# Kernel tuning notes

Measured on AMD Instinct MI355X. Metric: run time of the kernel, lower is better.

## Reference

```python
import jax, jax.numpy as jnp
import numpy as np

B = 16384      # batch
E = 128        # embed_dim
H = 256        # hidden_dim
OUT = 2        # output_dim
S = 32         # seq_length (decoder steps)
CAR = 8        # car_num


def setup_inputs() -> dict:
    key = jax.random.key(0)
    ks = jax.random.split(key, 17)
    def rn(k, shape, s=0.05):
        return jax.random.normal(k, shape, dtype=jnp.float32) * s
    return {
        "x": rn(ks[0], (B, 6 + CAR * 6), 1.0),
        "emb_mt_W": rn(ks[1], (E, 6)), "emb_mt_b": rn(ks[2], (E,)),
        "emb_v_W": rn(ks[3], (E, 6)), "emb_v_b": rn(ks[4], (E,)),
        "enc_Wih": rn(ks[5], (3 * H, E)), "enc_Whh": rn(ks[6], (3 * H, H)),
        "enc_bih": rn(ks[7], (3 * H,)), "enc_bhh": rn(ks[8], (3 * H,)),
        "dec_Wih": rn(ks[9], (3 * H, H)), "dec_Whh": rn(ks[10], (3 * H, H)),
        "dec_bih": rn(ks[11], (3 * H,)), "dec_bhh": rn(ks[12], (3 * H,)),
        "fc1_W": rn(ks[13], (H, H)), "fc1_b": rn(ks[14], (H,)),
        "fc2_W": rn(ks[15], (OUT, H)), "fc2_b": rn(ks[16], (OUT,)),
    }


def gru_cell(x, h, Wih, Whh, bih, bhh):
    # PyTorch GRU cell: r,z,n gate order
    gi = x @ Wih.T + bih          # [B, 3H]
    gh = h @ Whh.T + bhh          # [B, 3H]
    ir, iz, inn = jnp.split(gi, 3, axis=-1)
    hr, hz, hn = jnp.split(gh, 3, axis=-1)
    r = jax.nn.sigmoid(ir + hr)
    z = jax.nn.sigmoid(iz + hz)
    n = jnp.tanh(inn + r * hn)
    return (1.0 - z) * n + z * h


def reference(x, emb_mt_W, emb_mt_b, emb_v_W, emb_v_b,
              enc_Wih, enc_Whh, enc_bih, enc_bhh,
              dec_Wih, dec_Whh, dec_bih, dec_bhh,
              fc1_W, fc1_b, fc2_W, fc2_b):
    main_target = x[:, :6]                                  # [B,6]
    vehicles = x[:, 6:6 + CAR * 6].reshape(-1, CAR, 6)      # [B,CAR,6]
    # NOTE: original applies a random permutation over the CAR axis
    # (torch.randperm); we use the identity permutation for determinism,
    # the per-element math is identical.
    mt_emb = main_target @ emb_mt_W.T + emb_mt_b            # [B,E]
    v_emb = vehicles @ emb_v_W.T + emb_v_b                  # [B,CAR,E]
    seq = jnp.tanh(jnp.concatenate([v_emb, mt_emb[:, None, :]], axis=1))  # [B,CAR+1,E]

    h0 = jnp.zeros((x.shape[0], H), dtype=x.dtype)
    def enc_step(h, xt):
        return gru_cell(xt, h, enc_Wih, enc_Whh, enc_bih, enc_bhh), None
    h_enc, _ = jax.lax.scan(enc_step, h0, jnp.swapaxes(seq, 0, 1))  # [B,H]

    # decoder_input = encoder_output[:, -1] == final hidden (1-layer GRU)
    def dec_step(carry, _):
        dec_in, h = carry
        h = gru_cell(dec_in, h, dec_Wih, dec_Whh, dec_bih, dec_bhh)
        y = jnp.tanh(jax.nn.relu(h @ fc1_W.T + fc1_b) @ fc2_W.T + fc2_b)  # [B,OUT]
        return (h, h), y
    _, ys = jax.lax.scan(dec_step, (h_enc, h_enc), None, length=S)  # [S,B,OUT]
    return jnp.swapaxes(ys, 0, 1)  # [B,S,OUT]
```

## Files before the change

kernel.cpp:

```cpp
#include <hip/hip_runtime.h>
#include <math.h>
#include <stdint.h>

typedef _Float16 f16;
typedef _Float16 f16x8 __attribute__((ext_vector_type(8)));
typedef float    f32x16 __attribute__((ext_vector_type(16)));

#define NBLK 256
#define NTHR 512
#define MROW 64

#define FC1_F 512
#define FC2_F 640
#define ENC_F 656
#define TOT_F 1232
#define TOT_E (TOT_F*512)

#define MFMA32(a,b,c) __builtin_amdgcn_mfma_f32_32x32x16_f16((a),(b),(c),0,0,0)
#define VMW4()  asm volatile("s_waitcnt vmcnt(4)" ::: "memory")
#define LGKM0() asm volatile("s_waitcnt lgkmcnt(0)" ::: "memory")
#define BARR()  do { __builtin_amdgcn_s_barrier(); asm volatile("" ::: "memory"); } while(0)

__device__ __forceinline__ void gld16(const f16* g, f16* lds){
  __builtin_amdgcn_global_load_lds(
      (const __attribute__((address_space(1))) void*)(uintptr_t)(const void*)g,
      (__attribute__((address_space(3))) void*)(uint32_t)(uintptr_t)(void*)lds,
      16, 0, 0);
}

__device__ __forceinline__ float sigm(float v){
  return __fdividef(1.0f, 1.0f + __expf(-v));
}
__device__ __forceinline__ float tanh_f(float v){
  float t = fminf(v, 8.0f);
  float e = __expf(2.0f * t);
  return 1.0f - 2.0f * __fdividef(1.0f, e + 1.0f);
}
__device__ __forceinline__ int eX(int row, int k){ return row*128 + (k ^ ((row & 7) << 3)); }

__global__ void prep_pack(const float* __restrict__ eWih, const float* __restrict__ eWhh,
                          const float* __restrict__ dWih, const float* __restrict__ dWhh,
                          const float* __restrict__ f1W,  const float* __restrict__ f2W,
                          f16* __restrict__ ws16)
{
  int idx = blockIdx.x * 256 + threadIdx.x;
  if (idx >= TOT_E) return;
  int frag = idx >> 9;
  int lo   = idx & 511;
  int l    = lo >> 3;
  int jj   = lo & 7;
  int c32  = l & 31;
  int half = l >> 5;
  int kin  = half*8 + jj;
  float v = 0.0f;
  if (frag < FC1_F){
    int ct = frag >> 6, st = (frag >> 4) & 3, ks = frag & 15;
    int col = ct*32 + c32, k = ks*16 + kin;
    if      (st == 0) v = dWih[col*256 + k]        + dWhh[col*256 + k];
    else if (st == 1) v = dWih[(256+col)*256 + k]  + dWhh[(256+col)*256 + k];
    else if (st == 2) v = dWih[(512+col)*256 + k];
    else              v = dWhh[(512+col)*256 + k];
  } else if (frag < FC2_F){
    int f = frag - FC1_F, ct = f >> 4, ks = f & 15;
    int col = ct*32 + c32, k = ks*16 + kin;
    v = f1W[col*256 + k];
  } else if (frag < ENC_F){
    int ks = frag - FC2_F, k = ks*16 + kin;
    v = (c32 < 2) ? f2W[c32*256 + k] : 0.0f;
  } else {
    int f = frag - ENC_F, ct = f / 72, r = f % 72;
    int col = ct*32 + c32;
    if (r < 24){ int st = r >> 3, ks = r & 7;  v = eWih[(st*256 + col)*128 + ks*16 + kin]; }
    else { r -= 24; int st = r >> 4, ks = r & 15; v = eWhh[(st*256 + col)*256 + ks*16 + kin]; }
  }
  ws16[idx] = (f16)v;
}

__global__ __launch_bounds__(NTHR, 1)
void fused_net(const float* __restrict__ x,
               const float* __restrict__ emW, const float* __restrict__ emb_,
               const float* __restrict__ evW, const float* __restrict__ evb,
               const float* __restrict__ ebih, const float* __restrict__ ebhh,
               const float* __restrict__ dbih, const float* __restrict__ dbhh,
               const float* __restrict__ f1b, const float* __restrict__ f2b,
               const f16* __restrict__ ws16, float* __restrict__ out)
{
  __shared__ __align__(16) f16 H0[16384];
  __shared__ __align__(16) f16 H1[16384];
  __shared__ __align__(16) f16 stg[32768];
  __shared__ __align__(16) f16 xbuf[8192];

  const int tid  = threadIdx.x;
  const int r0   = blockIdx.x * MROW;
  const int l    = tid & 63;
  const int wu   = __builtin_amdgcn_readfirstlane(tid >> 6);
  const int c32  = l & 31;
  const int half = l >> 5;

  f16* hp = H0;
  f16* hq = H1;

  const int abase = c32*256 + ((half*8) ^ ((l & 7) << 3));
  const int xabase= c32*128 + ((half*8) ^ ((l & 7) << 3));
  const int colm  = wu*32 + c32;

  f16* slot0 = stg + wu*4096;

  const f16* wdecL = ws16 + (size_t)(wu*64)*512          + (size_t)l*8;
  const f16* wfc1L = ws16 + (size_t)(FC1_F + wu*16)*512  + (size_t)l*8;
  const f16* wfc2L = ws16 + (size_t)FC2_F*512            + (size_t)l*8;
  const f16* wencL = ws16 + (size_t)(ENC_F + wu*72)*512  + (size_t)l*8;

  auto enc_issue = [&](int n, int q){
    f16* d = slot0 + q*1024;
    const f16 *g0, *g1;
    if (n < 8)      {                g0 = wencL + (size_t)(     n)*512;  g1 = wencL + (size_t)( 8 + n)*512; }
    else if (n < 24){ int k = n-8;   g0 = wencL + (size_t)(24 + k)*512;  g1 = wencL + (size_t)(40 + k)*512; }
    else if (n < 28){ int j = 2*(n-24); g0 = wencL + (size_t)(16+j)*512; g1 = wencL + (size_t)(17+j)*512; }
    else            { int k = 2*(n-28); g0 = wencL + (size_t)(56+k)*512; g1 = wencL + (size_t)(57+k)*512; }
    gld16(g0, d); gld16(g1, d + 512);
  };
  auto dec_issue = [&](int n, int q){
    f16* d = slot0 + q*1024;
    const f16 *g0, *g1;
    if (n < 16)      {               g0 = wdecL + (size_t)(     n)*512;  g1 = wdecL + (size_t)(16 + n)*512; }
    else if (n < 32) { int k = n-16; g0 = wdecL + (size_t)(32 + k)*512;  g1 = wdecL + (size_t)(48 + k)*512; }
    else             { int f2 = 2*(n-32); g0 = wfc1L + (size_t)f2*512;   g1 = wfc1L + (size_t)(f2+1)*512; }
    gld16(g0, d); gld16(g1, d + 512);
  };

  enc_issue(0, 0); enc_issue(1, 1); enc_issue(2, 2);

  for (int i = tid; i < 16384; i += NTHR) H0[i] = (f16)0.0f;

  {
    const float ebr = ebih[colm]       + ebhh[colm];
    const float ebz = ebih[256 + colm] + ebhh[256 + colm];
    const float ebn = ebih[512 + colm];
    const float ebh = ebhh[512 + colm];

    #pragma unroll 1
    for (int t = 0; t < 9; ++t){
      {
        int e  = tid & 127;
        int rq = tid >> 7;
        const float* Wp = (t < 8) ? (evW + e*6) : (emW + e*6);
        float bb = (t < 8) ? evb[e] : emb_[e];
        float w0 = Wp[0], w1 = Wp[1], w2 = Wp[2], w3 = Wp[3], w4 = Wp[4], w5 = Wp[5];
        int xo = (t < 8) ? (6 + t*6) : 0;
        #pragma unroll 1
        for (int rr = 0; rr < 16; ++rr){
          int row = rq*16 + rr;
          const float* xs = x + (size_t)(r0 + row)*54 + xo;
          float a = bb + xs[0]*w0 + xs[1]*w1 + xs[2]*w2 + xs[3]*w3 + xs[4]*w4 + xs[5]*w5;
          xbuf[eX(row, e)] = (f16)tanh_f(a);
        }
      }
      LGKM0(); BARR();

      f32x16 rvv[2], zvv[2];
      {
        f32x16 aR[2], aZ[2];
        aR[0]=0.f; aR[1]=0.f; aZ[0]=0.f; aZ[1]=0.f;
        #pragma unroll 1
        for (int u = 0; u < 24; ++u){
          VMW4();
          int nn = u + 3;
          if (nn < 36) enc_issue(nn, nn & 3);
          else if (t < 8) enc_issue(nn - 36, nn & 3);
          else dec_issue(nn - 36, nn & 3);
          const f16* sp = slot0 + (u & 3)*1024;
          f16x8 b0 = *(const f16x8*)(sp + l*8);
          f16x8 b1 = *(const f16x8*)(sp + 512 + l*8);
          if (u < 8){
            int ao = xabase ^ (u << 4);
            f16x8 a0 = *(const f16x8*)(xbuf + ao);
            f16x8 a1 = *(const f16x8*)(xbuf + ao + 4096);
            aR[0]=MFMA32(a0,b0,aR[0]); aR[1]=MFMA32(a1,b0,aR[1]);
            aZ[0]=MFMA32(a0,b1,aZ[0]); aZ[1]=MFMA32(a1,b1,aZ[1]);
          } else {
            int ao = abase ^ ((u - 8) << 4);
            f16x8 a0 = *(const f16x8*)(hp + ao);
            f16x8 a1 = *(const f16x8*)(hp + ao + 8192);
            aR[0]=MFMA32(a0,b0,aR[0]); aR[1]=MFMA32(a1,b0,aR[1]);
            aZ[0]=MFMA32(a0,b1,aZ[0]); aZ[1]=MFMA32(a1,b1,aZ[1]);
          }
        }
        #pragma unroll
        for (int rt = 0; rt < 2; ++rt)
          #pragma unroll
          for (int rg = 0; rg < 16; ++rg){
            rvv[rt][rg] = sigm(aR[rt][rg] + ebr);
            zvv[rt][rg] = sigm(aZ[rt][rg] + ebz);
          }
      }
      {
        f32x16 aN[2], aH[2];
        aN[0]=0.f; aN[1]=0.f; aH[0]=0.f; aH[1]=0.f;
        #pragma unroll 1
        for (int m = 0; m < 12; ++m){
          int u = 24 + m;
          VMW4();
          int nn = u + 3;
          if (nn < 36) enc_issue(nn, nn & 3);
          else if (t < 8) enc_issue(nn - 36, nn & 3);
          else dec_issue(nn - 36, nn & 3);
          const f16* sp = slot0 + (u & 3)*1024;
          f16x8 b0 = *(const f16x8*)(sp + l*8);
          f16x8 b1 = *(const f16x8*)(sp + 512 + l*8);
          if (m < 4){
            int j = 2*m;
            int ao0 = xabase ^ (j << 4), ao1 = xabase ^ ((j+1) << 4);
            f16x8 a0 = *(const f16x8*)(xbuf + ao0);
            f16x8 a1 = *(const f16x8*)(xbuf + ao0 + 4096);
            aN[0]=MFMA32(a0,b0,aN[0]); aN[1]=MFMA32(a1,b0,aN[1]);
            f16x8 a2 = *(const f16x8*)(xbuf + ao1);
            f16x8 a3 = *(const f16x8*)(xbuf + ao1 + 4096);
            aN[0]=MFMA32(a2,b1,aN[0]); aN[1]=MFMA32(a3,b1,aN[1]);
          } else {
            int k = 2*(m-4);
            int ao0 = abase ^ (k << 4), ao1 = abase ^ ((k+1) << 4);
            f16x8 a0 = *(const f16x8*)(hp + ao0);
            f16x8 a1 = *(const f16x8*)(hp + ao0 + 8192);
            aH[0]=MFMA32(a0,b0,aH[0]); aH[1]=MFMA32(a1,b0,aH[1]);
            f16x8 a2 = *(const f16x8*)(hp + ao1);
            f16x8 a3 = *(const f16x8*)(hp + ao1 + 8192);
            aH[0]=MFMA32(a2,b1,aH[0]); aH[1]=MFMA32(a3,b1,aH[1]);
          }
        }
        #pragma unroll
        for (int rt = 0; rt < 2; ++rt){
          #pragma unroll
          for (int rg = 0; rg < 16; ++rg){
            int rr  = (rg & 3) + 8*(rg >> 2) + 4*half;
            int row = rt*32 + rr;
            int el  = row*256 + (colm ^ ((rr & 7) << 3));
            float nv = tanh_f(aN[rt][rg] + ebn + rvv[rt][rg]*(aH[rt][rg] + ebh));
            float ho = (float)hp[el];
            hq[el] = (f16)(nv + zvv[rt][rg]*(ho - nv));
          }
        }
      }
      LGKM0(); BARR();
      { f16* tmp = hp; hp = hq; hq = tmp; }
    }
  }

  const float dbr = dbih[colm]       + dbhh[colm];
  const float dbz = dbih[256 + colm] + dbhh[256 + colm];
  const float dbn = dbih[512 + colm];
  const float dbh = dbhh[512 + colm];
  const float f1bb = f1b[colm];
  const float f2bb = (c32 < 2) ? f2b[c32] : 0.0f;

  #pragma unroll 1
  for (int s = 0; s < 32; ++s){
    f32x16 rvv[2], zvv[2];
    {
      f32x16 aR[2], aZ[2];
      aR[0]=0.f; aR[1]=0.f; aZ[0]=0.f; aZ[1]=0.f;
      #pragma unroll 1
      for (int u = 0; u < 16; ++u){
        VMW4();
        int nn = u + 3;
        dec_issue(nn, nn & 3);
        const f16* sp = slot0 + (u & 3)*1024;
        f16x8 b0 = *(const f16x8*)(sp + l*8);
        f16x8 b1 = *(const f16x8*)(sp + 512 + l*8);
        int ao = abase ^ (u << 4);
        f16x8 a0 = *(const f16x8*)(hp + ao);
        f16x8 a1 = *(const f16x8*)(hp + ao + 8192);
        aR[0]=MFMA32(a0,b0,aR[0]); aR[1]=MFMA32(a1,b0,aR[1]);
        aZ[0]=MFMA32(a0,b1,aZ[0]); aZ[1]=MFMA32(a1,b1,aZ[1]);
      }
      #pragma unroll
      for (int rt = 0; rt < 2; ++rt)
        #pragma unroll
        for (int rg = 0; rg < 16; ++rg){
          rvv[rt][rg] = sigm(aR[rt][rg] + dbr);
          zvv[rt][rg] = sigm(aZ[rt][rg] + dbz);
        }
    }
    {
      f32x16 aN[2], aH[2];
      aN[0]=0.f; aN[1]=0.f; aH[0]=0.f; aH[1]=0.f;
      #pragma unroll 1
      for (int u = 16; u < 32; ++u){
        VMW4();
        int nn = u + 3;
        dec_issue(nn, nn & 3);
        const f16* sp = slot0 + (u & 3)*1024;
        f16x8 b0 = *(const f16x8*)(sp + l*8);
        f16x8 b1 = *(const f16x8*)(sp + 512 + l*8);
        int k = u - 16;
        int ao = abase ^ (k << 4);
        f16x8 a0 = *(const f16x8*)(hp + ao);
        f16x8 a1 = *(const f16x8*)(hp + ao + 8192);
        aN[0]=MFMA32(a0,b0,aN[0]); aN[1]=MFMA32(a1,b0,aN[1]);
        aH[0]=MFMA32(a0,b1,aH[0]); aH[1]=MFMA32(a1,b1,aH[1]);
      }
      #pragma unroll
      for (int rt = 0; rt < 2; ++rt){
        #pragma unroll
        for (int rg = 0; rg < 16; ++rg){
          int rr  = (rg & 3) + 8*(rg >> 2) + 4*half;
          int row = rt*32 + rr;
          int el  = row*256 + (colm ^ ((rr & 7) << 3));
          float nv = tanh_f(aN[rt][rg] + dbn + rvv[rt][rg]*(aH[rt][rg] + dbh));
          float ho = (float)hp[el];
          hq[el] = (f16)(nv + zvv[rt][rg]*(ho - nv));
        }
      }
    }
    LGKM0(); BARR();

    {
      f32x16 aF[2];
      aF[0]=0.f; aF[1]=0.f;
      #pragma unroll 1
      for (int f = 0; f < 8; ++f){
        VMW4();
        int nn = 35 + f;
        if (nn < 40) dec_issue(nn, nn & 3);
        else         dec_issue(nn - 40, nn & 3);
        const f16* sp = slot0 + (f & 3)*1024;
        f16x8 b0 = *(const f16x8*)(sp + l*8);
        f16x8 b1 = *(const f16x8*)(sp + 512 + l*8);
        int k0 = 2*f;
        int ao0 = abase ^ (k0 << 4), ao1 = abase ^ ((k0+1) << 4);
        f16x8 a0 = *(const f16x8*)(hq + ao0);
        f16x8 a1 = *(const f16x8*)(hq + ao0 + 8192);
        aF[0]=MFMA32(a0,b0,aF[0]); aF[1]=MFMA32(a1,b0,aF[1]);
        f16x8 a2 = *(const f16x8*)(hq + ao1);
        f16x8 a3 = *(const f16x8*)(hq + ao1 + 8192);
        aF[0]=MFMA32(a2,b1,aF[0]); aF[1]=MFMA32(a3,b1,aF[1]);
      }
      #pragma unroll
      for (int rt = 0; rt < 2; ++rt){
        #pragma unroll
        for (int rg = 0; rg < 16; ++rg){
          int rr  = (rg & 3) + 8*(rg >> 2) + 4*half;
          int row = rt*32 + rr;
          int el  = row*256 + (colm ^ ((rr & 7) << 3));
          hp[el] = (f16)fmaxf(aF[rt][rg] + f1bb, 0.0f);
        }
      }
    }
    LGKM0(); BARR();

    if (wu == 0){
      f32x16 a2r0 = 0.f, a2r1 = 0.f;
      #pragma unroll
      for (int ks = 0; ks < 16; ++ks){
        f16x8 bv = *(const f16x8*)(wfc2L + (size_t)ks*512);
        int ao = abase ^ (ks << 4);
        f16x8 a0 = *(const f16x8*)(hp + ao);
        f16x8 a1 = *(const f16x8*)(hp + ao + 8192);
        a2r0 = MFMA32(a0, bv, a2r0);
        a2r1 = MFMA32(a1, bv, a2r1);
      }
      if (c32 < 2){
        #pragma unroll
        for (int rg = 0; rg < 16; ++rg){
          int rr = (rg & 3) + 8*(rg >> 2) + 4*half;
          out[((size_t)(r0 + rr)*32 + s)*2 + c32]      = tanh_f(a2r0[rg] + f2bb);
          out[((size_t)(r0 + 32 + rr)*32 + s)*2 + c32] = tanh_f(a2r1[rg] + f2bb);
        }
      }
    }
    BARR();
    { f16* tmp = hp; hp = hq; hq = tmp; }
  }
}

extern "C" void kernel_launch(void* const* d_in, const int* in_sizes, int n_in,
                              void* d_out, int out_size, void* d_ws, size_t ws_size,
                              hipStream_t stream)
{
  (void)in_sizes; (void)n_in; (void)out_size; (void)ws_size;
  const float* x    = (const float*)d_in[0];
  const float* emW  = (const float*)d_in[1];
  const float* emb_ = (const float*)d_in[2];
  const float* evW  = (const float*)d_in[3];
  const float* evb  = (const float*)d_in[4];
  const float* eWih = (const float*)d_in[5];
  const float* eWhh = (const float*)d_in[6];
  const float* ebih = (const float*)d_in[7];
  const float* ebhh = (const float*)d_in[8];
  const float* dWih = (const float*)d_in[9];
  const float* dWhh = (const float*)d_in[10];
  const float* dbih = (const float*)d_in[11];
  const float* dbhh = (const float*)d_in[12];
  const float* f1W  = (const float*)d_in[13];
  const float* f1b  = (const float*)d_in[14];
  const float* f2W  = (const float*)d_in[15];
  const float* f2b  = (const float*)d_in[16];
  float* out = (float*)d_out;
  f16* ws16 = (f16*)d_ws;

  prep_pack<<<(TOT_E + 255)/256, 256, 0, stream>>>(eWih, eWhh, dWih, dWhh, f1W, f2W, ws16);
  fused_net<<<NBLK, NTHR, 0, stream>>>(x, emW, emb_, evW, evb, ebih, ebhh,
                                       dbih, dbhh, f1b, f2b, ws16, out);
}
```

Measured before the change: 904.1 us.

## Stream weights directly into registers instead of LDS staging ring

Replaces the per-wave global_load_lds staging ring and its vmcnt waits with direct global-to-register loads of weight fragments, kept in a 4-deep register queue and prefetched four steps ahead in fully unrolled loops. This frees the 64KB stg LDS buffer and removes the LDS read round-trip for B fragments. The fc2 head is also split across two waves, each handling 32 rows, and its weights are prefetched in groups of four. The register queue and full unrolling raise VGPR pressure, and waits now depend on compiler-inserted vmcnt placement rather than explicit control.

```diff
diff --git a/kernel.cpp b/kernel.cpp
--- a/kernel.cpp
+++ b/kernel.cpp
@@ -17,16 +17,8 @@
 #define TOT_E (TOT_F*512)
 
 #define MFMA32(a,b,c) __builtin_amdgcn_mfma_f32_32x32x16_f16((a),(b),(c),0,0,0)
-#define VMW4()  asm volatile("s_waitcnt vmcnt(4)" ::: "memory")
 #define LGKM0() asm volatile("s_waitcnt lgkmcnt(0)" ::: "memory")
 #define BARR()  do { __builtin_amdgcn_s_barrier(); asm volatile("" ::: "memory"); } while(0)
-
-__device__ __forceinline__ void gld16(const f16* g, f16* lds){
-  __builtin_amdgcn_global_load_lds(
-      (const __attribute__((address_space(1))) void*)(uintptr_t)(const void*)g,
-      (__attribute__((address_space(3))) void*)(uint32_t)(uintptr_t)(void*)lds,
-      16, 0, 0);
-}
 
 __device__ __forceinline__ float sigm(float v){
   return __fdividef(1.0f, 1.0f + __expf(-v));
@@ -87,7 +79,6 @@
 {
   __shared__ __align__(16) f16 H0[16384];
   __shared__ __align__(16) f16 H1[16384];
-  __shared__ __align__(16) f16 stg[32768];
   __shared__ __align__(16) f16 xbuf[8192];
 
   const int tid  = threadIdx.x;
@@ -96,40 +87,37 @@
   const int wu   = __builtin_amdgcn_readfirstlane(tid >> 6);
   const int c32  = l & 31;
   const int half = l >> 5;
+  const int lo8  = l << 3;
 
   f16* hp = H0;
   f16* hq = H1;
 
   const int abase = c32*256 + ((half*8) ^ ((l & 7) << 3));
-  const int xabase= c32*128 + ((half*8) ^ ((l & 7) << 3));
+  const int xab   = c32*128 + ((half*8) ^ ((l & 7) << 3));
   const int colm  = wu*32 + c32;
 
-  f16* slot0 = stg + wu*4096;
-
-  const f16* wdecL = ws16 + (size_t)(wu*64)*512          + (size_t)l*8;
-  const f16* wfc1L = ws16 + (size_t)(FC1_F + wu*16)*512  + (size_t)l*8;
-  const f16* wfc2L = ws16 + (size_t)FC2_F*512            + (size_t)l*8;
-  const f16* wencL = ws16 + (size_t)(ENC_F + wu*72)*512  + (size_t)l*8;
-
-  auto enc_issue = [&](int n, int q){
-    f16* d = slot0 + q*1024;
-    const f16 *g0, *g1;
-    if (n < 8)      {                g0 = wencL + (size_t)(     n)*512;  g1 = wencL + (size_t)( 8 + n)*512; }
-    else if (n < 24){ int k = n-8;   g0 = wencL + (size_t)(24 + k)*512;  g1 = wencL + (size_t)(40 + k)*512; }
-    else if (n < 28){ int j = 2*(n-24); g0 = wencL + (size_t)(16+j)*512; g1 = wencL + (size_t)(17+j)*512; }
-    else            { int k = 2*(n-28); g0 = wencL + (size_t)(56+k)*512; g1 = wencL + (size_t)(57+k)*512; }
-    gld16(g0, d); gld16(g1, d + 512);
+  const f16* wdec = ws16 + (size_t)(wu*64)*512;
+  const f16* wfc1 = ws16 + (size_t)(FC1_F + wu*16)*512;
+  const f16* wfc2 = ws16 + (size_t)FC2_F*512;
+  const f16* wenc = ws16 + (size_t)(ENC_F + wu*72)*512;
+
+  #define LDW(base, frag) (*(const f16x8*)((base) + (size_t)(frag)*512 + lo8))
+
+  auto encb = [&](int n, f16x8* d){
+    if (n < 8)      {                  d[0] = LDW(wenc, n);        d[1] = LDW(wenc, 8 + n); }
+    else if (n < 24){ int k = n - 8;   d[0] = LDW(wenc, 24 + k);   d[1] = LDW(wenc, 40 + k); }
+    else if (n < 28){ int j = 2*(n-24);d[0] = LDW(wenc, 16 + j);   d[1] = LDW(wenc, 17 + j); }
+    else            { int k = 2*(n-28);d[0] = LDW(wenc, 56 + k);   d[1] = LDW(wenc, 57 + k); }
   };
-  auto dec_issue = [&](int n, int q){
-    f16* d = slot0 + q*1024;
-    const f16 *g0, *g1;
-    if (n < 16)      {               g0 = wdecL + (size_t)(     n)*512;  g1 = wdecL + (size_t)(16 + n)*512; }
-    else if (n < 32) { int k = n-16; g0 = wdecL + (size_t)(32 + k)*512;  g1 = wdecL + (size_t)(48 + k)*512; }
-    else             { int f2 = 2*(n-32); g0 = wfc1L + (size_t)f2*512;   g1 = wfc1L + (size_t)(f2+1)*512; }
-    gld16(g0, d); gld16(g1, d + 512);
+  auto decb = [&](int n, f16x8* d){
+    if (n < 16)      {               d[0] = LDW(wdec, n);        d[1] = LDW(wdec, 16 + n); }
+    else if (n < 32) { int k = n-16; d[0] = LDW(wdec, 32 + k);   d[1] = LDW(wdec, 48 + k); }
+    else             { int f = n-32; d[0] = LDW(wfc1, 2*f);      d[1] = LDW(wfc1, 2*f + 1); }
   };
 
-  enc_issue(0, 0); enc_issue(1, 1); enc_issue(2, 2);
+  f16x8 bq[4][2];
+  #pragma unroll
+  for (int p = 0; p < 4; ++p) encb(p, bq[p]);
 
   for (int i = tid; i < 16384; i += NTHR) H0[i] = (f16)0.0f;
 
@@ -141,13 +129,14 @@
 
     #pragma unroll 1
     for (int t = 0; t < 9; ++t){
+      const bool tlt8 = (t < 8);
       {
         int e  = tid & 127;
         int rq = tid >> 7;
-        const float* Wp = (t < 8) ? (evW + e*6) : (emW + e*6);
-        float bb = (t < 8) ? evb[e] : emb_[e];
+        const float* Wp = tlt8 ? (evW + e*6) : (emW + e*6);
+        float bb = tlt8 ? evb[e] : emb_[e];
         float w0 = Wp[0], w1 = Wp[1], w2 = Wp[2], w3 = Wp[3], w4 = Wp[4], w5 = Wp[5];
-        int xo = (t < 8) ? (6 + t*6) : 0;
+        int xo = tlt8 ? (6 + t*6) : 0;
         #pragma unroll 1
         for (int rr = 0; rr < 16; ++rr){
           int row = rq*16 + rr;
@@ -162,18 +151,13 @@
       {
         f32x16 aR[2], aZ[2];
         aR[0]=0.f; aR[1]=0.f; aZ[0]=0.f; aZ[1]=0.f;
-        #pragma unroll 1
+        #pragma unroll
         for (int u = 0; u < 24; ++u){
-          VMW4();
-          int nn = u + 3;
-          if (nn < 36) enc_issue(nn, nn & 3);
-          else if (t < 8) enc_issue(nn - 36, nn & 3);
-          else dec_issue(nn - 36, nn & 3);
-          const f16* sp = slot0 + (u & 3)*1024;
-          f16x8 b0 = *(const f16x8*)(sp + l*8);
-          f16x8 b1 = *(const f16x8*)(sp + 512 + l*8);
+          f16x8 b0 = bq[u & 3][0];
+          f16x8 b1 = bq[u & 3][1];
+          encb(u + 4, bq[u & 3]);
           if (u < 8){
-            int ao = xabase ^ (u << 4);
+            int ao = xab ^ (u << 4);
             f16x8 a0 = *(const f16x8*)(xbuf + ao);
             f16x8 a1 = *(const f16x8*)(xbuf + ao + 4096);
             aR[0]=MFMA32(a0,b0,aR[0]); aR[1]=MFMA32(a1,b0,aR[1]);
@@ -197,20 +181,16 @@
       {
         f32x16 aN[2], aH[2];
         aN[0]=0.f; aN[1]=0.f; aH[0]=0.f; aH[1]=0.f;
-        #pragma unroll 1
+        #pragma unroll
         for (int m = 0; m < 12; ++m){
-          int u = 24 + m;
-          VMW4();
-          int nn = u + 3;
-          if (nn < 36) enc_issue(nn, nn & 3);
-          else if (t < 8) enc_issue(nn - 36, nn & 3);
-          else dec_issue(nn - 36, nn & 3);
-          const f16* sp = slot0 + (u & 3)*1024;
-          f16x8 b0 = *(const f16x8*)(sp + l*8);
-          f16x8 b1 = *(const f16x8*)(sp + 512 + l*8);
+          f16x8 b0 = bq[m & 3][0];
+          f16x8 b1 = bq[m & 3][1];
+          if (m < 8) encb(28 + m, bq[m & 3]);
+          else if (tlt8) encb(m - 8, bq[m & 3]);
+          else decb(m - 8, bq[m & 3]);
           if (m < 4){
             int j = 2*m;
-            int ao0 = xabase ^ (j << 4), ao1 = xabase ^ ((j+1) << 4);
+            int ao0 = xab ^ (j << 4), ao1 = xab ^ ((j+1) << 4);
             f16x8 a0 = *(const f16x8*)(xbuf + ao0);
             f16x8 a1 = *(const f16x8*)(xbuf + ao0 + 4096);
             aN[0]=MFMA32(a0,b0,aN[0]); aN[1]=MFMA32(a1,b0,aN[1]);
@@ -259,14 +239,11 @@
     {
       f32x16 aR[2], aZ[2];
       aR[0]=0.f; aR[1]=0.f; aZ[0]=0.f; aZ[1]=0.f;
-      #pragma unroll 1
+      #pragma unroll
       for (int u = 0; u < 16; ++u){
-        VMW4();
-        int nn = u + 3;
-        dec_issue(nn, nn & 3);
-        const f16* sp = slot0 + (u & 3)*1024;
-        f16x8 b0 = *(const f16x8*)(sp + l*8);
-        f16x8 b1 = *(const f16x8*)(sp + 512 + l*8);
+        f16x8 b0 = bq[u & 3][0];
+        f16x8 b1 = bq[u & 3][1];
+        decb(u + 4, bq[u & 3]);
         int ao = abase ^ (u << 4);
         f16x8 a0 = *(const f16x8*)(hp + ao);
         f16x8 a1 = *(const f16x8*)(hp + ao + 8192);
@@ -284,14 +261,11 @@
     {
       f32x16 aN[2], aH[2];
       aN[0]=0.f; aN[1]=0.f; aH[0]=0.f; aH[1]=0.f;
-      #pragma unroll 1
+      #pragma unroll
       for (int u = 16; u < 32; ++u){
-        VMW4();
-        int nn = u + 3;
-        dec_issue(nn, nn & 3);
-        const f16* sp = slot0 + (u & 3)*1024;
-        f16x8 b0 = *(const f16x8*)(sp + l*8);
-        f16x8 b1 = *(const f16x8*)(sp + 512 + l*8);
+        f16x8 b0 = bq[u & 3][0];
+        f16x8 b1 = bq[u & 3][1];
+        decb(u + 4, bq[u & 3]);
         int k = u - 16;
         int ao = abase ^ (k << 4);
         f16x8 a0 = *(const f16x8*)(hp + ao);
@@ -317,15 +291,13 @@
     {
       f32x16 aF[2];
       aF[0]=0.f; aF[1]=0.f;
-      #pragma unroll 1
-      for (int f = 0; f < 8; ++f){
-        VMW4();
-        int nn = 35 + f;
-        if (nn < 40) dec_issue(nn, nn & 3);
-        else         dec_issue(nn - 40, nn & 3);
-        const f16* sp = slot0 + (f & 3)*1024;
-        f16x8 b0 = *(const f16x8*)(sp + l*8);
-        f16x8 b1 = *(const f16x8*)(sp + 512 + l*8);
+      #pragma unroll
+      for (int u = 32; u < 40; ++u){
+        f16x8 b0 = bq[u & 3][0];
+        f16x8 b1 = bq[u & 3][1];
+        if (u + 4 < 40) decb(u + 4, bq[u & 3]);
+        else            decb(u - 36, bq[u & 3]);
+        int f = u - 32;
         int k0 = 2*f;
         int ao0 = abase ^ (k0 << 4), ao1 = abase ^ ((k0+1) << 4);
         f16x8 a0 = *(const f16x8*)(hq + ao0);
@@ -348,29 +320,41 @@
     }
     LGKM0(); BARR();
 
-    if (wu == 0){
-      f32x16 a2r0 = 0.f, a2r1 = 0.f;
-      #pragma unroll
-      for (int ks = 0; ks < 16; ++ks){
-        f16x8 bv = *(const f16x8*)(wfc2L + (size_t)ks*512);
-        int ao = abase ^ (ks << 4);
-        f16x8 a0 = *(const f16x8*)(hp + ao);
-        f16x8 a1 = *(const f16x8*)(hp + ao + 8192);
-        a2r0 = MFMA32(a0, bv, a2r0);
-        a2r1 = MFMA32(a1, bv, a2r1);
+    if (wu < 2){
+      f32x16 a2 = 0.f;
+      f16x8 c0 = LDW(wfc2, 0), c1 = LDW(wfc2, 1), c2 = LDW(wfc2, 2), c3 = LDW(wfc2, 3);
+      const int rb = wu * 8192;
+      #pragma unroll
+      for (int g = 0; g < 4; ++g){
+        f16x8 u0 = c0, u1 = c1, u2 = c2, u3 = c3;
+        if (g < 3){
+          c0 = LDW(wfc2, (g+1)*4 + 0);
+          c1 = LDW(wfc2, (g+1)*4 + 1);
+          c2 = LDW(wfc2, (g+1)*4 + 2);
+          c3 = LDW(wfc2, (g+1)*4 + 3);
+        }
+        int kb = g*4;
+        f16x8 a0 = *(const f16x8*)(hp + ((abase + rb) ^ ((kb + 0) << 4)));
+        a2 = MFMA32(a0, u0, a2);
+        f16x8 a1 = *(const f16x8*)(hp + ((abase + rb) ^ ((kb + 1) << 4)));
+        a2 = MFMA32(a1, u1, a2);
+        f16x8 av2 = *(const f16x8*)(hp + ((abase + rb) ^ ((kb + 2) << 4)));
+        a2 = MFMA32(av2, u2, a2);
+        f16x8 a3 = *(const f16x8*)(hp + ((abase + rb) ^ ((kb + 3) << 4)));
+        a2 = MFMA32(a3, u3, a2);
       }
       if (c32 < 2){
         #pragma unroll
         for (int rg = 0; rg < 16; ++rg){
           int rr = (rg & 3) + 8*(rg >> 2) + 4*half;
-          out[((size_t)(r0 + rr)*32 + s)*2 + c32]      = tanh_f(a2r0[rg] + f2bb);
-          out[((size_t)(r0 + 32 + rr)*32 + s)*2 + c32] = tanh_f(a2r1[rg] + f2bb);
+          out[((size_t)(r0 + wu*32 + rr)*32 + s)*2 + c32] = tanh_f(a2[rg] + f2bb);
         }
       }
     }
     BARR();
     { f16* tmp = hp; hp = hq; hq = tmp; }
   }
+  #undef LDW
 }
 
 extern "C" void kernel_launch(void* const* d_in, const int* in_sizes, int n_in,
```

Result: slower. 1.659 ms (+83.4%).

## Repack weight fragments contiguously per stream and split fc2 across two waves

Applied to the files above, without the earlier changes.

Reorders the packed fp16 weight fragments so that every pipelined load is a contiguous pair at base+n*1024, which replaces the branchy address computation with a single issue helper. Loops gain partial or full unrolling. The fc2 output projection is split across two waves, one per 32-row half, instead of running on one wave. The barrier after fc2 is moved to sit between the decoder r/z and n phases, which shortens the tail but changes the hazard ordering on hp and hq and could create a race.

```diff
diff --git a/kernel.cpp b/kernel.cpp
--- a/kernel.cpp
+++ b/kernel.cpp
@@ -10,9 +10,8 @@
 #define NTHR 512
 #define MROW 64
 
-#define FC1_F 512
-#define FC2_F 640
-#define ENC_F 656
+#define ENCS 640
+#define FC2S 1216
 #define TOT_F 1232
 #define TOT_E (TOT_F*512)
 
@@ -53,25 +52,28 @@
   int half = l >> 5;
   int kin  = half*8 + jj;
   float v = 0.0f;
-  if (frag < FC1_F){
-    int ct = frag >> 6, st = (frag >> 4) & 3, ks = frag & 15;
-    int col = ct*32 + c32, k = ks*16 + kin;
-    if      (st == 0) v = dWih[col*256 + k]        + dWhh[col*256 + k];
-    else if (st == 1) v = dWih[(256+col)*256 + k]  + dWhh[(256+col)*256 + k];
-    else if (st == 2) v = dWih[(512+col)*256 + k];
-    else              v = dWhh[(512+col)*256 + k];
-  } else if (frag < FC2_F){
-    int f = frag - FC1_F, ct = f >> 4, ks = f & 15;
-    int col = ct*32 + c32, k = ks*16 + kin;
-    v = f1W[col*256 + k];
-  } else if (frag < ENC_F){
-    int ks = frag - FC2_F, k = ks*16 + kin;
+  if (frag < ENCS){
+    int ct = frag / 80, r80 = frag % 80, n = r80 >> 1, j = r80 & 1;
+    int col = ct*32 + c32;
+    if (n < 16){ int k = n*16 + kin;
+      v = (j == 0) ? (dWih[col*256 + k]       + dWhh[col*256 + k])
+                   : (dWih[(256+col)*256 + k] + dWhh[(256+col)*256 + k]);
+    } else if (n < 32){ int k = (n-16)*16 + kin;
+      v = (j == 0) ? dWih[(512+col)*256 + k] : dWhh[(512+col)*256 + k];
+    } else { int ks = (n-32)*2 + j; int k = ks*16 + kin;
+      v = f1W[col*256 + k];
+    }
+  } else if (frag < FC2S){
+    int f = frag - ENCS;
+    int ct = f / 72, r = f % 72, n = r >> 1, j = r & 1;
+    int col = ct*32 + c32;
+    if (n < 8)       { int k = n*16 + kin;       v = eWih[(j*256 + col)*128 + k]; }
+    else if (n < 24) { int k = (n-8)*16 + kin;   v = eWhh[(j*256 + col)*256 + k]; }
+    else if (n < 28) { int ks = (n-24)*2 + j;    v = eWih[(512 + col)*128 + ks*16 + kin]; }
+    else             { int ks = (n-28)*2 + j;    v = eWhh[(512 + col)*256 + ks*16 + kin]; }
+  } else {
+    int ks = frag - FC2S; int k = ks*16 + kin;
     v = (c32 < 2) ? f2W[c32*256 + k] : 0.0f;
-  } else {
-    int f = frag - ENC_F, ct = f / 72, r = f % 72;
-    int col = ct*32 + c32;
-    if (r < 24){ int st = r >> 3, ks = r & 7;  v = eWih[(st*256 + col)*128 + ks*16 + kin]; }
-    else { r -= 24; int st = r >> 4, ks = r & 15; v = eWhh[(st*256 + col)*256 + ks*16 + kin]; }
   }
   ws16[idx] = (f16)v;
 }
@@ -96,40 +98,29 @@
   const int wu   = __builtin_amdgcn_readfirstlane(tid >> 6);
   const int c32  = l & 31;
   const int half = l >> 5;
+  const int lo8  = l << 3;
 
   f16* hp = H0;
   f16* hq = H1;
 
   const int abase = c32*256 + ((half*8) ^ ((l & 7) << 3));
-  const int xabase= c32*128 + ((half*8) ^ ((l & 7) << 3));
+  const int xab   = c32*128 + ((half*8) ^ ((l & 7) << 3));
   const int colm  = wu*32 + c32;
 
   f16* slot0 = stg + wu*4096;
 
-  const f16* wdecL = ws16 + (size_t)(wu*64)*512          + (size_t)l*8;
-  const f16* wfc1L = ws16 + (size_t)(FC1_F + wu*16)*512  + (size_t)l*8;
-  const f16* wfc2L = ws16 + (size_t)FC2_F*512            + (size_t)l*8;
-  const f16* wencL = ws16 + (size_t)(ENC_F + wu*72)*512  + (size_t)l*8;
-
-  auto enc_issue = [&](int n, int q){
+  const f16* gdec = ws16 + (size_t)(wu*80)*512          + lo8;
+  const f16* genc = ws16 + (size_t)(ENCS + wu*72)*512   + lo8;
+  const f16* gfc2 = ws16 + (size_t)FC2S*512             + lo8;
+
+  auto issue = [&](const f16* sb, int n, int q){
     f16* d = slot0 + q*1024;
-    const f16 *g0, *g1;
-    if (n < 8)      {                g0 = wencL + (size_t)(     n)*512;  g1 = wencL + (size_t)( 8 + n)*512; }
-    else if (n < 24){ int k = n-8;   g0 = wencL + (size_t)(24 + k)*512;  g1 = wencL + (size_t)(40 + k)*512; }
-    else if (n < 28){ int j = 2*(n-24); g0 = wencL + (size_t)(16+j)*512; g1 = wencL + (size_t)(17+j)*512; }
-    else            { int k = 2*(n-28); g0 = wencL + (size_t)(56+k)*512; g1 = wencL + (size_t)(57+k)*512; }
-    gld16(g0, d); gld16(g1, d + 512);
+    const f16* g = sb + (size_t)n*1024;
+    gld16(g, d);
+    gld16(g + 512, d + 512);
   };
-  auto dec_issue = [&](int n, int q){
-    f16* d = slot0 + q*1024;
-    const f16 *g0, *g1;
-    if (n < 16)      {               g0 = wdecL + (size_t)(     n)*512;  g1 = wdecL + (size_t)(16 + n)*512; }
-    else if (n < 32) { int k = n-16; g0 = wdecL + (size_t)(32 + k)*512;  g1 = wdecL + (size_t)(48 + k)*512; }
-    else             { int f2 = 2*(n-32); g0 = wfc1L + (size_t)f2*512;   g1 = wfc1L + (size_t)(f2+1)*512; }
-    gld16(g0, d); gld16(g1, d + 512);
-  };
-
-  enc_issue(0, 0); enc_issue(1, 1); enc_issue(2, 2);
+
+  issue(genc, 0, 0); issue(genc, 1, 1); issue(genc, 2, 2);
 
   for (int i = tid; i < 16384; i += NTHR) H0[i] = (f16)0.0f;
 
@@ -141,13 +132,14 @@
 
     #pragma unroll 1
     for (int t = 0; t < 9; ++t){
+      const bool tlt8 = (t < 8);
       {
         int e  = tid & 127;
         int rq = tid >> 7;
-        const float* Wp = (t < 8) ? (evW + e*6) : (emW + e*6);
-        float bb = (t < 8) ? evb[e] : emb_[e];
+        const float* Wp = tlt8 ? (evW + e*6) : (emW + e*6);
+        float bb = tlt8 ? evb[e] : emb_[e];
         float w0 = Wp[0], w1 = Wp[1], w2 = Wp[2], w3 = Wp[3], w4 = Wp[4], w5 = Wp[5];
-        int xo = (t < 8) ? (6 + t*6) : 0;
+        int xo = tlt8 ? (6 + t*6) : 0;
         #pragma unroll 1
         for (int rr = 0; rr < 16; ++rr){
           int row = rq*16 + rr;
@@ -162,18 +154,15 @@
       {
         f32x16 aR[2], aZ[2];
         aR[0]=0.f; aR[1]=0.f; aZ[0]=0.f; aZ[1]=0.f;
-        #pragma unroll 1
+        #pragma unroll 4
         for (int u = 0; u < 24; ++u){
           VMW4();
-          int nn = u + 3;
-          if (nn < 36) enc_issue(nn, nn & 3);
-          else if (t < 8) enc_issue(nn - 36, nn & 3);
-          else dec_issue(nn - 36, nn & 3);
+          issue(genc, u + 3, (u + 3) & 3);
           const f16* sp = slot0 + (u & 3)*1024;
-          f16x8 b0 = *(const f16x8*)(sp + l*8);
-          f16x8 b1 = *(const f16x8*)(sp + 512 + l*8);
+          f16x8 b0 = *(const f16x8*)(sp + lo8);
+          f16x8 b1 = *(const f16x8*)(sp + 512 + lo8);
           if (u < 8){
-            int ao = xabase ^ (u << 4);
+            int ao = xab ^ (u << 4);
             f16x8 a0 = *(const f16x8*)(xbuf + ao);
             f16x8 a1 = *(const f16x8*)(xbuf + ao + 4096);
             aR[0]=MFMA32(a0,b0,aR[0]); aR[1]=MFMA32(a1,b0,aR[1]);
@@ -197,20 +186,20 @@
       {
         f32x16 aN[2], aH[2];
         aN[0]=0.f; aN[1]=0.f; aH[0]=0.f; aH[1]=0.f;
-        #pragma unroll 1
+        #pragma unroll
         for (int m = 0; m < 12; ++m){
           int u = 24 + m;
           VMW4();
           int nn = u + 3;
-          if (nn < 36) enc_issue(nn, nn & 3);
-          else if (t < 8) enc_issue(nn - 36, nn & 3);
-          else dec_issue(nn - 36, nn & 3);
+          if (nn < 36)      issue(genc, nn, nn & 3);
+          else if (tlt8)    issue(genc, nn - 36, nn & 3);
+          else              issue(gdec, nn - 36, nn & 3);
           const f16* sp = slot0 + (u & 3)*1024;
-          f16x8 b0 = *(const f16x8*)(sp + l*8);
-          f16x8 b1 = *(const f16x8*)(sp + 512 + l*8);
+          f16x8 b0 = *(const f16x8*)(sp + lo8);
+          f16x8 b1 = *(const f16x8*)(sp + 512 + lo8);
           if (m < 4){
             int j = 2*m;
-            int ao0 = xabase ^ (j << 4), ao1 = xabase ^ ((j+1) << 4);
+            int ao0 = xab ^ (j << 4), ao1 = xab ^ ((j+1) << 4);
             f16x8 a0 = *(const f16x8*)(xbuf + ao0);
             f16x8 a1 = *(const f16x8*)(xbuf + ao0 + 4096);
             aN[0]=MFMA32(a0,b0,aN[0]); aN[1]=MFMA32(a1,b0,aN[1]);
@@ -259,14 +248,13 @@
     {
       f32x16 aR[2], aZ[2];
       aR[0]=0.f; aR[1]=0.f; aZ[0]=0.f; aZ[1]=0.f;
-      #pragma unroll 1
+      #pragma unroll 4
       for (int u = 0; u < 16; ++u){
         VMW4();
-        int nn = u + 3;
-        dec_issue(nn, nn & 3);
+        issue(gdec, u + 3, (u + 3) & 3);
         const f16* sp = slot0 + (u & 3)*1024;
-        f16x8 b0 = *(const f16x8*)(sp + l*8);
-        f16x8 b1 = *(const f16x8*)(sp + 512 + l*8);
+        f16x8 b0 = *(const f16x8*)(sp + lo8);
+        f16x8 b1 = *(const f16x8*)(sp + 512 + lo8);
         int ao = abase ^ (u << 4);
         f16x8 a0 = *(const f16x8*)(hp + ao);
         f16x8 a1 = *(const f16x8*)(hp + ao + 8192);
@@ -281,17 +269,18 @@
           zvv[rt][rg] = sigm(aZ[rt][rg] + dbz);
         }
     }
+    BARR();
+
     {
       f32x16 aN[2], aH[2];
       aN[0]=0.f; aN[1]=0.f; aH[0]=0.f; aH[1]=0.f;
-      #pragma unroll 1
+      #pragma unroll 4
       for (int u = 16; u < 32; ++u){
         VMW4();
-        int nn = u + 3;
-        dec_issue(nn, nn & 3);
+        issue(gdec, u + 3, (u + 3) & 3);
         const f16* sp = slot0 + (u & 3)*1024;
-        f16x8 b0 = *(const f16x8*)(sp + l*8);
-        f16x8 b1 = *(const f16x8*)(sp + 512 + l*8);
+        f16x8 b0 = *(const f16x8*)(sp + lo8);
+        f16x8 b1 = *(const f16x8*)(sp + 512 + lo8);
         int k = u - 16;
         int ao = abase ^ (k << 4);
         f16x8 a0 = *(const f16x8*)(hp + ao);
@@ -317,15 +306,15 @@
     {
       f32x16 aF[2];
       aF[0]=0.f; aF[1]=0.f;
-      #pragma unroll 1
+      #pragma unroll
       for (int f = 0; f < 8; ++f){
         VMW4();
         int nn = 35 + f;
-        if (nn < 40) dec_issue(nn, nn & 3);
-        else         dec_issue(nn - 40, nn & 3);
+        if (nn < 40) issue(gdec, nn, nn & 3);
+        else         issue(gdec, nn - 40, nn & 3);
         const f16* sp = slot0 + (f & 3)*1024;
-        f16x8 b0 = *(const f16x8*)(sp + l*8);
-        f16x8 b1 = *(const f16x8*)(sp + 512 + l*8);
+        f16x8 b0 = *(const f16x8*)(sp + lo8);
+        f16x8 b1 = *(const f16x8*)(sp + 512 + lo8);
         int k0 = 2*f;
         int ao0 = abase ^ (k0 << 4), ao1 = abase ^ ((k0+1) << 4);
         f16x8 a0 = *(const f16x8*)(hq + ao0);
@@ -348,27 +337,23 @@
     }
     LGKM0(); BARR();
 
-    if (wu == 0){
-      f32x16 a2r0 = 0.f, a2r1 = 0.f;
+    if (wu < 2){
+      f32x16 a2 = 0.f;
+      const int rb = wu * 8192;
       #pragma unroll
       for (int ks = 0; ks < 16; ++ks){
-        f16x8 bv = *(const f16x8*)(wfc2L + (size_t)ks*512);
-        int ao = abase ^ (ks << 4);
-        f16x8 a0 = *(const f16x8*)(hp + ao);
-        f16x8 a1 = *(const f16x8*)(hp + ao + 8192);
-        a2r0 = MFMA32(a0, bv, a2r0);
-        a2r1 = MFMA32(a1, bv, a2r1);
+        f16x8 bv = *(const f16x8*)(gfc2 + (size_t)ks*512);
+        f16x8 a0 = *(const f16x8*)(hp + ((abase + rb) ^ (ks << 4)));
+        a2 = MFMA32(a0, bv, a2);
       }
       if (c32 < 2){
         #pragma unroll
         for (int rg = 0; rg < 16; ++rg){
           int rr = (rg & 3) + 8*(rg >> 2) + 4*half;
-          out[((size_t)(r0 + rr)*32 + s)*2 + c32]      = tanh_f(a2r0[rg] + f2bb);
-          out[((size_t)(r0 + 32 + rr)*32 + s)*2 + c32] = tanh_f(a2r1[rg] + f2bb);
-        }
-      }
-    }
-    BARR();
+          out[((size_t)(r0 + wu*32 + rr)*32 + s)*2 + c32] = tanh_f(a2[rg] + f2bb);
+        }
+      }
+    }
     { f16* tmp = hp; hp = hq; hq = tmp; }
   }
 }
```

New measurement: 748.4 us. 17.2% less time.
